# Kernel optimization log

Measured on AMD Instinct MI355X. Metric: run time of the kernel, lower is better.

Reference implementation:

```python
import jax, jax.numpy as jnp
import numpy as np

B, S, D, H = 2, 4096, 512, 8
HD = D // H

def setup_inputs() -> dict:
    key = jax.random.key(0)
    ks = jax.random.split(key, 9)
    s = 1.0 / np.sqrt(D)
    inp = {"x": jax.random.normal(ks[0], (B, S, D), dtype=jnp.float32)}
    names = ["Wq", "Wk", "Wv", "Wo"]
    for i, n in enumerate(names):
        inp[n] = jax.random.uniform(ks[1 + 2 * i], (D, D), jnp.float32, -s, s)
        inp["b" + n[1]] = jax.random.uniform(ks[2 + 2 * i], (D,), jnp.float32, -s, s)
    return inp


def reference(x, Wq, bq, Wk, bk, Wv, bv, Wo, bo):
    # projections (torch Linear: x @ W.T + b)
    def proj(W, b):
        return (x @ W.T + b).reshape(B, S, H, HD).transpose(0, 2, 1, 3)  # [B,H,S,HD]
    q = proj(Wq, bq)
    k = proj(Wk, bk)
    v = proj(Wv, bv)
    scores = jnp.einsum("bhqd,bhkd->bhqk", q, k) / np.sqrt(HD).astype(np.float32)
    attn = jax.nn.softmax(scores, axis=-1)
    out = jnp.einsum("bhqk,bhkd->bhqd", attn, v)
    out = out.transpose(0, 2, 1, 3).reshape(B, S, D)
    return out @ Wo.T + bo
```

## Files before the change

### kernel.cpp

```cpp
#include <hip/hip_runtime.h>
#include <hip/hip_bf16.h>

#define DEV __device__ __forceinline__

typedef float f32x4 __attribute__((ext_vector_type(4)));
typedef float f32x16 __attribute__((ext_vector_type(16)));
typedef __bf16 bf16x8 __attribute__((ext_vector_type(8)));
typedef unsigned short u16;
typedef unsigned short u16x8 __attribute__((ext_vector_type(8)));

DEV u16 f2bf(float f) {
    __bf16 h = (__bf16)f;
    return __builtin_bit_cast(u16, h);
}
DEV float bf2f(u16 u) {
    __bf16 h = __builtin_bit_cast(__bf16, u);
    return (float)h;
}

DEV f32x4 mfma16(bf16x8 a, bf16x8 b, f32x4 c) {
    return __builtin_amdgcn_mfma_f32_16x16x32_bf16(a, b, c, 0, 0, 0);
}
DEV f32x16 mfma32(bf16x8 a, bf16x8 b, f32x16 c) {
    return __builtin_amdgcn_mfma_f32_32x32x16_bf16(a, b, c, 0, 0, 0);
}

DEV unsigned cvtpk(float lo, float hi) {
    unsigned r;
    asm("v_cvt_pk_bf16_f32 %0, %1, %2" : "=v"(r) : "v"(lo), "v"(hi));
    return r;
}
DEV void pswap(unsigned& a, unsigned& b) {
    asm volatile("v_permlane32_swap_b32 %0, %1" : "+v"(a), "+v"(b));
}

DEV int kidx(int row, int col) { return row * 64 + (col ^ ((row & 7) << 3)); }
DEV int xidx(int row, int col) { return row * 32 + (col ^ ((row & 3) << 3)); }

__global__ __launch_bounds__(256) void cvt_kernel(
    const float* __restrict__ x, const float* __restrict__ wq,
    const float* __restrict__ wk, const float* __restrict__ wv,
    const float* __restrict__ wo,
    u16* __restrict__ xb, u16* __restrict__ wb)
{
    size_t e0 = ((size_t)blockIdx.x * 256 + threadIdx.x) * 8;
    const float* src; u16* dst; size_t off;
    if (e0 < 4194304) { src = x; dst = xb; off = e0; }
    else {
        size_t r = e0 - 4194304;
        int seg = (int)(r >> 18);
        src = (seg == 0) ? wq : (seg == 1) ? wk : (seg == 2) ? wv : wo;
        dst = wb + (size_t)seg * 262144;
        off = r & 262143;
    }
    f32x4 a = *(const f32x4*)(src + off);
    f32x4 b = *(const f32x4*)(src + off + 4);
    u16x8 o;
    #pragma unroll
    for (int i = 0; i < 4; ++i) { o[i] = f2bf(a[i]); o[i + 4] = f2bf(b[i]); }
    *(u16x8*)(dst + off) = o;
}

__global__ __launch_bounds__(256) void proj_qkv_kernel(
    const u16* __restrict__ xb, const u16* __restrict__ wb,
    const float* __restrict__ bq, const float* __restrict__ bk, const float* __restrict__ bv,
    u16* __restrict__ qo, u16* __restrict__ ko, u16* __restrict__ vo)
{
    __shared__ u16 Xs[128 * 32], Wsh[128 * 32];
    const int tid = threadIdx.x;
    const int m0 = blockIdx.x * 128, n0 = blockIdx.y * 128, z = blockIdx.z;
    const u16* W = wb + (size_t)z * 262144;
    const float* bias = (z == 0) ? bq : (z == 1) ? bk : bv;

    const int lane = tid & 63, wv = tid >> 6;
    const int g = lane >> 4, c = lane & 15;
    const int wr = wv >> 1, wcl = wv & 1;
    const int srow = tid >> 1, scol = (tid & 1) * 16;

    f32x4 acc[4][4] = {};

    for (int k0 = 0; k0 < 512; k0 += 32) {
        const u16* xp = xb + (size_t)(m0 + srow) * 512 + k0 + scol;
        const u16* wp = W  + (size_t)(n0 + srow) * 512 + k0 + scol;
        uint4 xa = *(const uint4*)xp, xa2 = *(const uint4*)(xp + 8);
        uint4 wa = *(const uint4*)wp, wa2 = *(const uint4*)(wp + 8);
        __syncthreads();
        *(uint4*)&Xs[xidx(srow, scol)]      = xa;
        *(uint4*)&Xs[xidx(srow, scol + 8)]  = xa2;
        *(uint4*)&Wsh[xidx(srow, scol)]     = wa;
        *(uint4*)&Wsh[xidx(srow, scol + 8)] = wa2;
        __syncthreads();

        bf16x8 af[4], bfr[4];
        #pragma unroll
        for (int mt = 0; mt < 4; ++mt)
            af[mt] = *(const bf16x8*)&Xs[xidx(wr * 64 + mt * 16 + c, g * 8)];
        #pragma unroll
        for (int nt = 0; nt < 4; ++nt)
            bfr[nt] = *(const bf16x8*)&Wsh[xidx(wcl * 64 + nt * 16 + c, g * 8)];

        if (z < 2) {
            #pragma unroll
            for (int mt = 0; mt < 4; ++mt)
                #pragma unroll
                for (int nt = 0; nt < 4; ++nt)
                    acc[mt][nt] = mfma16(af[mt], bfr[nt], acc[mt][nt]);
        } else {
            #pragma unroll
            for (int mt = 0; mt < 4; ++mt)
                #pragma unroll
                for (int nt = 0; nt < 4; ++nt)
                    acc[mt][nt] = mfma16(bfr[nt], af[mt], acc[mt][nt]);
        }
    }

    if (z < 2) {
        const float scale = (z == 0) ? 0.18033688011112042f : 1.0f;
        u16* outp = (z == 0) ? qo : ko;
        float bn[4];
        #pragma unroll
        for (int nt = 0; nt < 4; ++nt) bn[nt] = bias[n0 + wcl * 64 + nt * 16 + c];
        #pragma unroll
        for (int mt = 0; mt < 4; ++mt)
            #pragma unroll
            for (int r = 0; r < 4; ++r) {
                int mg = m0 + wr * 64 + mt * 16 + g * 4 + r;
                int b = mg >> 12, s = mg & 4095;
                #pragma unroll
                for (int nt = 0; nt < 4; ++nt) {
                    int ng = n0 + wcl * 64 + nt * 16 + c;
                    int h = ng >> 6, d = ng & 63;
                    outp[((size_t)(b * 8 + h) * 4096 + s) * 64 + d] =
                        f2bf((acc[mt][nt][r] + bn[nt]) * scale);
                }
            }
    } else {
        #pragma unroll
        for (int nt = 0; nt < 4; ++nt)
            #pragma unroll
            for (int r = 0; r < 4; ++r) {
                int ng = n0 + wcl * 64 + nt * 16 + g * 4 + r;
                int h = ng >> 6, d = ng & 63;
                float bnr = bias[ng];
                #pragma unroll
                for (int mt = 0; mt < 4; ++mt) {
                    int mg = m0 + wr * 64 + mt * 16 + c;
                    int b = mg >> 12, s = mg & 4095;
                    vo[((size_t)(b * 8 + h) * 64 + d) * 4096 + s] =
                        f2bf(acc[mt][nt][r] + bnr);
                }
            }
    }
}

__global__ __launch_bounds__(256, 4) void flash_attn_kernel(
    const u16* __restrict__ Q, const u16* __restrict__ K,
    const u16* __restrict__ Vt, u16* __restrict__ Opart, float* __restrict__ lbuf)
{
    __shared__ u16 Ks[2][64 * 64];
    __shared__ u16 Vs[2][64 * 64];

    const int tid = threadIdx.x;
    const int bh = blockIdx.y;
    const int q0 = blockIdx.x * 128;
    const int half = blockIdx.z;
    const int kvbase = half * 2048;
    const int lane = tid & 63, wv = tid >> 6;
    const int l31 = lane & 31, hi = lane >> 5;

    const u16* Qb = Q  + (size_t)bh * (4096 * 64);
    const u16* Kb = K  + (size_t)bh * (4096 * 64);
    const u16* Vb = Vt + (size_t)bh * (64 * 4096);

    u16x8 onesu;
    #pragma unroll
    for (int i = 0; i < 8; ++i) onesu[i] = 0x3F80;
    const bf16x8 ones = __builtin_bit_cast(bf16x8, onesu);

    const int qrow = q0 + wv * 32 + l31;
    bf16x8 qf[4];
    #pragma unroll
    for (int ds = 0; ds < 4; ++ds)
        qf[ds] = *(const bf16x8*)(Qb + (size_t)qrow * 64 + ds * 16 + hi * 8);

    f32x16 oA[2] = {};
    f32x16 oL = {};

    const int sr = tid >> 3, sc8 = (tid & 7) * 8;
    const u16* kp0 = Kb + (size_t)(kvbase + sr) * 64 + sc8;
    const u16* vp0 = Vb + (size_t)sr * 4096 + kvbase + sc8;

    uint4 rk0 = *(const uint4*)(kp0);
    uint4 rk1 = *(const uint4*)(kp0 + 32 * 64);
    uint4 rv0 = *(const uint4*)(vp0);
    uint4 rv1 = *(const uint4*)(vp0 + 32 * 4096);

    for (int t = 0; t < 32; ++t) {
        const int p = t & 1;
        *(uint4*)&Ks[p][kidx(sr, sc8)]      = rk0;
        *(uint4*)&Ks[p][kidx(sr + 32, sc8)] = rk1;
        *(uint4*)&Vs[p][kidx(sr, sc8)]      = rv0;
        *(uint4*)&Vs[p][kidx(sr + 32, sc8)] = rv1;
        if (t < 31) {
            const int kv1 = (t + 1) * 64;
            rk0 = *(const uint4*)(kp0 + (size_t)kv1 * 64);
            rk1 = *(const uint4*)(kp0 + (size_t)(kv1 + 32) * 64);
            rv0 = *(const uint4*)(vp0 + kv1);
            rv1 = *(const uint4*)(vp0 + 32 * 4096 + kv1);
        }
        __syncthreads();

        #pragma unroll
        for (int ct = 0; ct < 2; ++ct) {
            f32x16 sA = {};
            __builtin_amdgcn_s_setprio(1);
            #pragma unroll
            for (int ds = 0; ds < 4; ++ds) {
                bf16x8 kf = *(const bf16x8*)&Ks[p][kidx(ct * 32 + l31, ds * 16 + hi * 8)];
                sA = mfma32(kf, qf[ds], sA);
            }
            __builtin_amdgcn_s_setprio(0);

            float pv[16];
            #pragma unroll
            for (int r = 0; r < 16; ++r)
                pv[r] = __builtin_amdgcn_exp2f(sA[r]);

            unsigned a0 = cvtpk(pv[0],  pv[1]),  a1 = cvtpk(pv[2],  pv[3]);
            unsigned b0 = cvtpk(pv[4],  pv[5]),  b1 = cvtpk(pv[6],  pv[7]);
            pswap(a0, b0); pswap(a1, b1);
            uint4 w0; w0.x = a0; w0.y = a1; w0.z = b0; w0.w = b1;
            bf16x8 pfa = __builtin_bit_cast(bf16x8, w0);
            unsigned c0 = cvtpk(pv[8],  pv[9]),  c1 = cvtpk(pv[10], pv[11]);
            unsigned d0 = cvtpk(pv[12], pv[13]), d1 = cvtpk(pv[14], pv[15]);
            pswap(c0, d0); pswap(c1, d1);
            uint4 w1; w1.x = c0; w1.y = c1; w1.z = d0; w1.w = d1;
            bf16x8 pfb = __builtin_bit_cast(bf16x8, w1);

            __builtin_amdgcn_s_setprio(1);
            oL = mfma32(ones, pfa, oL);
            oL = mfma32(ones, pfb, oL);
            #pragma unroll
            for (int hf = 0; hf < 2; ++hf) {
                const int ks = 2 * ct + hf;
                const bf16x8 pfx = hf ? pfb : pfa;
                bf16x8 vf0 = *(const bf16x8*)&Vs[p][kidx(l31,      ks * 16 + hi * 8)];
                bf16x8 vf1 = *(const bf16x8*)&Vs[p][kidx(32 + l31, ks * 16 + hi * 8)];
                oA[0] = mfma32(vf0, pfx, oA[0]);
                oA[1] = mfma32(vf1, pfx, oA[1]);
            }
            __builtin_amdgcn_s_setprio(0);
        }
    }

    if (hi == 0)
        lbuf[(size_t)(half * 16 + bh) * 4096 + qrow] = oL[0];

    const int b = bh >> 3, h = bh & 7;
    u16* Ob = Opart + (size_t)half * 4194304 +
              ((size_t)(b * 4096 + qrow)) * 512 + h * 64;
    #pragma unroll
    for (int dt = 0; dt < 2; ++dt) {
        const f32x16 oa = dt ? oA[1] : oA[0];
        #pragma unroll
        for (int qd = 0; qd < 4; ++qd) {
            unsigned w0 = cvtpk(oa[qd * 4 + 0], oa[qd * 4 + 1]);
            unsigned w1 = cvtpk(oa[qd * 4 + 2], oa[qd * 4 + 3]);
            uint2 st; st.x = w0; st.y = w1;
            *(uint2*)(Ob + dt * 32 + qd * 8 + hi * 4) = st;
        }
    }
}

__global__ __launch_bounds__(256) void combine_kernel(
    const u16* __restrict__ Opart, const float* __restrict__ lbuf,
    u16* __restrict__ obuf)
{
    const size_t idx8 = ((size_t)blockIdx.x * 256 + threadIdx.x) * 8;
    const int m = (int)(idx8 >> 9);
    const int hd = (int)(idx8 & 511);
    const int b = m >> 12, s = m & 4095, h = hd >> 6;
    const int bh = b * 8 + h;
    const float la = lbuf[(size_t)bh * 4096 + s];
    const float lb = lbuf[(size_t)(16 + bh) * 4096 + s];
    const float inv = 1.0f / (la + lb);
    u16x8 a = *(const u16x8*)(Opart + idx8);
    u16x8 c = *(const u16x8*)(Opart + 4194304 + idx8);
    u16x8 o;
    #pragma unroll
    for (int i = 0; i < 8; ++i)
        o[i] = f2bf((bf2f(a[i]) + bf2f(c[i])) * inv);
    *(u16x8*)(obuf + idx8) = o;
}

__global__ __launch_bounds__(256) void out_proj_kernel(
    const u16* __restrict__ Ob, const u16* __restrict__ Wob,
    const float* __restrict__ bo, float* __restrict__ out)
{
    __shared__ u16 Xs[128 * 32], Wsh[128 * 32];
    const int tid = threadIdx.x;
    const int m0 = blockIdx.x * 128, n0 = blockIdx.y * 128;

    const int lane = tid & 63, wv = tid >> 6;
    const int g = lane >> 4, c = lane & 15;
    const int wr = wv >> 1, wcl = wv & 1;
    const int srow = tid >> 1, scol = (tid & 1) * 16;

    f32x4 acc[4][4] = {};

    for (int k0 = 0; k0 < 512; k0 += 32) {
        const u16* xp = Ob  + (size_t)(m0 + srow) * 512 + k0 + scol;
        const u16* wp = Wob + (size_t)(n0 + srow) * 512 + k0 + scol;
        uint4 xa = *(const uint4*)xp, xa2 = *(const uint4*)(xp + 8);
        uint4 wa = *(const uint4*)wp, wa2 = *(const uint4*)(wp + 8);
        __syncthreads();
        *(uint4*)&Xs[xidx(srow, scol)]      = xa;
        *(uint4*)&Xs[xidx(srow, scol + 8)]  = xa2;
        *(uint4*)&Wsh[xidx(srow, scol)]     = wa;
        *(uint4*)&Wsh[xidx(srow, scol + 8)] = wa2;
        __syncthreads();

        bf16x8 af[4], bfr[4];
        #pragma unroll
        for (int mt = 0; mt < 4; ++mt)
            af[mt] = *(const bf16x8*)&Xs[xidx(wr * 64 + mt * 16 + c, g * 8)];
        #pragma unroll
        for (int nt = 0; nt < 4; ++nt)
            bfr[nt] = *(const bf16x8*)&Wsh[xidx(wcl * 64 + nt * 16 + c, g * 8)];

        #pragma unroll
        for (int mt = 0; mt < 4; ++mt)
            #pragma unroll
            for (int nt = 0; nt < 4; ++nt)
                acc[mt][nt] = mfma16(bfr[nt], af[mt], acc[mt][nt]);
    }

    #pragma unroll
    for (int nt = 0; nt < 4; ++nt) {
        f32x4 bi = *(const f32x4*)&bo[n0 + wcl * 64 + nt * 16 + g * 4];
        #pragma unroll
        for (int mt = 0; mt < 4; ++mt) {
            int m = m0 + wr * 64 + mt * 16 + c;
            f32x4 v;
            #pragma unroll
            for (int r = 0; r < 4; ++r) v[r] = acc[mt][nt][r] + bi[r];
            *(f32x4*)&out[(size_t)m * 512 + n0 + wcl * 64 + nt * 16 + g * 4] = v;
        }
    }
}

extern "C" void kernel_launch(void* const* d_in, const int* in_sizes, int n_in,
                              void* d_out, int out_size, void* d_ws, size_t ws_size,
                              hipStream_t stream) {
    const float* x  = (const float*)d_in[0];
    const float* Wq = (const float*)d_in[1];
    const float* bq = (const float*)d_in[2];
    const float* Wk = (const float*)d_in[3];
    const float* bk = (const float*)d_in[4];
    const float* Wv = (const float*)d_in[5];
    const float* bv = (const float*)d_in[6];
    const float* Wo = (const float*)d_in[7];
    const float* bo = (const float*)d_in[8];
    float* out = (float*)d_out;

    const size_t NQKV = (size_t)2 * 8 * 4096 * 64;
    u16* qw = (u16*)d_ws;
    u16* kw = qw + NQKV;
    u16* vw = kw + NQKV;
    u16* wbuf = vw + NQKV;
    float* lbuf = (float*)(wbuf + 4 * 262144);
    u16* xbuf = (u16*)(lbuf + 2 * 16 * 4096);
    u16* opart = (u16*)d_out;
    u16* obuf = qw;

    cvt_kernel<<<2560, 256, 0, stream>>>(x, Wq, Wk, Wv, Wo, xbuf, wbuf);
    proj_qkv_kernel<<<dim3(64, 4, 3), 256, 0, stream>>>(xbuf, wbuf, bq, bk, bv, qw, kw, vw);
    flash_attn_kernel<<<dim3(32, 16, 2), 256, 0, stream>>>(qw, kw, vw, opart, lbuf);
    combine_kernel<<<2048, 256, 0, stream>>>(opart, lbuf, obuf);
    out_proj_kernel<<<dim3(64, 4), 256, 0, stream>>>(obuf, wbuf + 3 * 262144, bo, out);
}
```

Before: 147.1 us.

## Stage GEMM and attention tiles via direct global-to-LDS loads with double buffering

```diff
diff --git a/kernel.cpp b/kernel.cpp
--- a/kernel.cpp
+++ b/kernel.cpp
@@ -32,6 +32,13 @@
 }
 DEV void pswap(unsigned& a, unsigned& b) {
     asm volatile("v_permlane32_swap_b32 %0, %1" : "+v"(a), "+v"(b));
+}
+
+DEV void gll16(const u16* g, u16* l) {
+    __builtin_amdgcn_global_load_lds(
+        (const __attribute__((address_space(1))) unsigned int*)g,
+        (__attribute__((address_space(3))) unsigned int*)l,
+        16, 0, 0);
 }
 
 DEV int kidx(int row, int col) { return row * 64 + (col ^ ((row & 7) << 3)); }
@@ -66,7 +73,7 @@
     const float* __restrict__ bq, const float* __restrict__ bk, const float* __restrict__ bv,
     u16* __restrict__ qo, u16* __restrict__ ko, u16* __restrict__ vo)
 {
-    __shared__ u16 Xs[128 * 32], Wsh[128 * 32];
+    __shared__ u16 Xs[2][128 * 32], Wsh[2][128 * 32];
     const int tid = threadIdx.x;
     const int m0 = blockIdx.x * 128, n0 = blockIdx.y * 128, z = blockIdx.z;
     const u16* W = wb + (size_t)z * 262144;
@@ -75,29 +82,39 @@
     const int lane = tid & 63, wv = tid >> 6;
     const int g = lane >> 4, c = lane & 15;
     const int wr = wv >> 1, wcl = wv & 1;
-    const int srow = tid >> 1, scol = (tid & 1) * 16;
+
+    const int r0 = wv * 32 + (lane >> 2);
+    const int csz = (((lane & 3) ^ ((lane >> 2) & 3)) << 3);
+    const u16* xg0 = xb + (size_t)(m0 + r0) * 512 + csz;
+    const u16* xg1 = xg0 + 16 * 512;
+    const u16* wg0 = W + (size_t)(n0 + r0) * 512 + csz;
+    const u16* wg1 = wg0 + 16 * 512;
 
     f32x4 acc[4][4] = {};
 
-    for (int k0 = 0; k0 < 512; k0 += 32) {
-        const u16* xp = xb + (size_t)(m0 + srow) * 512 + k0 + scol;
-        const u16* wp = W  + (size_t)(n0 + srow) * 512 + k0 + scol;
-        uint4 xa = *(const uint4*)xp, xa2 = *(const uint4*)(xp + 8);
-        uint4 wa = *(const uint4*)wp, wa2 = *(const uint4*)(wp + 8);
+    gll16(xg0, &Xs[0][wv * 1024]);
+    gll16(xg1, &Xs[0][wv * 1024 + 512]);
+    gll16(wg0, &Wsh[0][wv * 1024]);
+    gll16(wg1, &Wsh[0][wv * 1024 + 512]);
+
+    for (int it = 0; it < 16; ++it) {
+        const int p = it & 1;
         __syncthreads();
-        *(uint4*)&Xs[xidx(srow, scol)]      = xa;
-        *(uint4*)&Xs[xidx(srow, scol + 8)]  = xa2;
-        *(uint4*)&Wsh[xidx(srow, scol)]     = wa;
-        *(uint4*)&Wsh[xidx(srow, scol + 8)] = wa2;
-        __syncthreads();
+        if (it < 15) {
+            const int kn = (it + 1) * 32;
+            gll16(xg0 + kn, &Xs[p ^ 1][wv * 1024]);
+            gll16(xg1 + kn, &Xs[p ^ 1][wv * 1024 + 512]);
+            gll16(wg0 + kn, &Wsh[p ^ 1][wv * 1024]);
+            gll16(wg1 + kn, &Wsh[p ^ 1][wv * 1024 + 512]);
+        }
 
         bf16x8 af[4], bfr[4];
         #pragma unroll
         for (int mt = 0; mt < 4; ++mt)
-            af[mt] = *(const bf16x8*)&Xs[xidx(wr * 64 + mt * 16 + c, g * 8)];
+            af[mt] = *(const bf16x8*)&Xs[p][xidx(wr * 64 + mt * 16 + c, g * 8)];
         #pragma unroll
         for (int nt = 0; nt < 4; ++nt)
-            bfr[nt] = *(const bf16x8*)&Wsh[xidx(wcl * 64 + nt * 16 + c, g * 8)];
+            bfr[nt] = *(const bf16x8*)&Wsh[p][xidx(wcl * 64 + nt * 16 + c, g * 8)];
 
         if (z < 2) {
             #pragma unroll
@@ -186,29 +203,29 @@
     f32x16 oA[2] = {};
     f32x16 oL = {};
 
-    const int sr = tid >> 3, sc8 = (tid & 7) * 8;
-    const u16* kp0 = Kb + (size_t)(kvbase + sr) * 64 + sc8;
-    const u16* vp0 = Vb + (size_t)sr * 4096 + kvbase + sc8;
-
-    uint4 rk0 = *(const uint4*)(kp0);
-    uint4 rk1 = *(const uint4*)(kp0 + 32 * 64);
-    uint4 rv0 = *(const uint4*)(vp0);
-    uint4 rv1 = *(const uint4*)(vp0 + 32 * 4096);
+    const int kr = wv * 16 + (lane >> 3);
+    const int csz = (((lane & 7) ^ (lane >> 3)) << 3);
+    const u16* kg0 = Kb + (size_t)(kvbase + kr) * 64 + csz;
+    const u16* kg1 = kg0 + 8 * 64;
+    const u16* vg0 = Vb + (size_t)kr * 4096 + kvbase + csz;
+    const u16* vg1 = vg0 + 8 * 4096;
+
+    gll16(kg0, &Ks[0][wv * 1024]);
+    gll16(kg1, &Ks[0][wv * 1024 + 512]);
+    gll16(vg0, &Vs[0][wv * 1024]);
+    gll16(vg1, &Vs[0][wv * 1024 + 512]);
 
     for (int t = 0; t < 32; ++t) {
         const int p = t & 1;
-        *(uint4*)&Ks[p][kidx(sr, sc8)]      = rk0;
-        *(uint4*)&Ks[p][kidx(sr + 32, sc8)] = rk1;
-        *(uint4*)&Vs[p][kidx(sr, sc8)]      = rv0;
-        *(uint4*)&Vs[p][kidx(sr + 32, sc8)] = rv1;
+        __syncthreads();
         if (t < 31) {
-            const int kv1 = (t + 1) * 64;
-            rk0 = *(const uint4*)(kp0 + (size_t)kv1 * 64);
-            rk1 = *(const uint4*)(kp0 + (size_t)(kv1 + 32) * 64);
-            rv0 = *(const uint4*)(vp0 + kv1);
-            rv1 = *(const uint4*)(vp0 + 32 * 4096 + kv1);
-        }
-        __syncthreads();
+            const size_t ko = (size_t)(t + 1) * 4096;
+            const size_t vofs = (size_t)(t + 1) * 64;
+            gll16(kg0 + ko, &Ks[p ^ 1][wv * 1024]);
+            gll16(kg1 + ko, &Ks[p ^ 1][wv * 1024 + 512]);
+            gll16(vg0 + vofs, &Vs[p ^ 1][wv * 1024]);
+            gll16(vg1 + vofs, &Vs[p ^ 1][wv * 1024 + 512]);
+        }
 
         #pragma unroll
         for (int ct = 0; ct < 2; ++ct) {
@@ -297,36 +314,46 @@
     const u16* __restrict__ Ob, const u16* __restrict__ Wob,
     const float* __restrict__ bo, float* __restrict__ out)
 {
-    __shared__ u16 Xs[128 * 32], Wsh[128 * 32];
+    __shared__ u16 Xs[2][128 * 32], Wsh[2][128 * 32];
     const int tid = threadIdx.x;
     const int m0 = blockIdx.x * 128, n0 = blockIdx.y * 128;
 
     const int lane = tid & 63, wv = tid >> 6;
     const int g = lane >> 4, c = lane & 15;
     const int wr = wv >> 1, wcl = wv & 1;
-    const int srow = tid >> 1, scol = (tid & 1) * 16;
+
+    const int r0 = wv * 32 + (lane >> 2);
+    const int csz = (((lane & 3) ^ ((lane >> 2) & 3)) << 3);
+    const u16* xg0 = Ob + (size_t)(m0 + r0) * 512 + csz;
+    const u16* xg1 = xg0 + 16 * 512;
+    const u16* wg0 = Wob + (size_t)(n0 + r0) * 512 + csz;
+    const u16* wg1 = wg0 + 16 * 512;
 
     f32x4 acc[4][4] = {};
 
-    for (int k0 = 0; k0 < 512; k0 += 32) {
-        const u16* xp = Ob  + (size_t)(m0 + srow) * 512 + k0 + scol;
-        const u16* wp = Wob + (size_t)(n0 + srow) * 512 + k0 + scol;
-        uint4 xa = *(const uint4*)xp, xa2 = *(const uint4*)(xp + 8);
-        uint4 wa = *(const uint4*)wp, wa2 = *(const uint4*)(wp + 8);
+    gll16(xg0, &Xs[0][wv * 1024]);
+    gll16(xg1, &Xs[0][wv * 1024 + 512]);
+    gll16(wg0, &Wsh[0][wv * 1024]);
+    gll16(wg1, &Wsh[0][wv * 1024 + 512]);
+
+    for (int it = 0; it < 16; ++it) {
+        const int p = it & 1;
         __syncthreads();
-        *(uint4*)&Xs[xidx(srow, scol)]      = xa;
-        *(uint4*)&Xs[xidx(srow, scol + 8)]  = xa2;
-        *(uint4*)&Wsh[xidx(srow, scol)]     = wa;
-        *(uint4*)&Wsh[xidx(srow, scol + 8)] = wa2;
-        __syncthreads();
+        if (it < 15) {
+            const int kn = (it + 1) * 32;
+            gll16(xg0 + kn, &Xs[p ^ 1][wv * 1024]);
+            gll16(xg1 + kn, &Xs[p ^ 1][wv * 1024 + 512]);
+            gll16(wg0 + kn, &Wsh[p ^ 1][wv * 1024]);
+            gll16(wg1 + kn, &Wsh[p ^ 1][wv * 1024 + 512]);
+        }
 
         bf16x8 af[4], bfr[4];
         #pragma unroll
         for (int mt = 0; mt < 4; ++mt)
-            af[mt] = *(const bf16x8*)&Xs[xidx(wr * 64 + mt * 16 + c, g * 8)];
+            af[mt] = *(const bf16x8*)&Xs[p][xidx(wr * 64 + mt * 16 + c, g * 8)];
         #pragma unroll
         for (int nt = 0; nt < 4; ++nt)
-            bfr[nt] = *(const bf16x8*)&Wsh[xidx(wcl * 64 + nt * 16 + c, g * 8)];
+            bfr[nt] = *(const bf16x8*)&Wsh[p][xidx(wcl * 64 + nt * 16 + c, g * 8)];
 
         #pragma unroll
         for (int mt = 0; mt < 4; ++mt)
```

Result: faster. 140.2 us (-4.7%).
